# Kernel optimization log

Measured on AMD Instinct MI355X. Metric: run time of the kernel, lower is better.

Reference implementation:

```python
import jax, jax.numpy as jnp
import numpy as np

B = 4_000_000

# physical constants from initBatteryParams
R_ = 8.3144621
F_ = 96487.0
ALPHA = 0.5
SN = 0.0002
SP = 0.0002
KN = 20000.0
KP = 20000.0
VOL = 2.2e-05
VOLS = 0.1 * VOL
VOLB = VOL - VOLS
TO = 10.0
TSN = 90.0
TSP = 90.0
U0P = 4.03
U0N = 0.01
QMAX_BASE = 10000.0
RO_BASE = 10.0
T_DIFFUSION = 7.0e6  # repo default; attribute used in getNextState
DT = 1.0


def setup_inputs() -> dict:
    key = jax.random.key(0)
    ks = jax.random.split(key, 12)
    qMax = 1.4 * jnp.ones((B,), jnp.float32)   # 14000/qMaxBASE
    Ro = 0.015 * jnp.ones((B,), jnp.float32)   # 0.15/RoBASE
    # physically plausible initial state (get_initial_state) + small noise
    qM = qMax * QMAX_BASE  # [B]
    Tb = 292.1 + 0.5 * jax.random.normal(ks[0], (B, 1), jnp.float32)
    Vo = 0.01 * jax.random.uniform(ks[1], (B, 1), jnp.float32)
    Vsn = 0.01 * jax.random.uniform(ks[2], (B, 1), jnp.float32)
    Vsp = 0.01 * jax.random.uniform(ks[3], (B, 1), jnp.float32)
    jitter = lambda k: 1.0 + 0.01 * jax.random.normal(k, (B, 1), jnp.float32)
    qnB = (qM * 0.6 * VOLB / VOL)[:, None] * jitter(ks[4])
    qnS = (qM * 0.6 * VOLS / VOL)[:, None] * jitter(ks[5])
    qpB = (qM * 0.4 * VOLB / VOL)[:, None] * jitter(ks[6])
    qpS = (qM * 0.4 * VOLS / VOL)[:, None] * jitter(ks[7])
    states = jnp.concatenate([Tb, Vo, Vsn, Vsp, qnB, qnS, qpB, qpS], axis=1)
    inputs = 1.0 + 2.0 * jax.random.uniform(ks[8], (B, 1), jnp.float32)  # current [A]
    kw = jax.random.split(ks[9], 8)
    return {
        "inputs": inputs, "states": states, "qMax": qMax, "Ro": Ro,
        "Wp0": 0.5 * jax.random.normal(kw[0], (8, 1), jnp.float32),
        "bp0": 0.1 * jax.random.normal(kw[1], (8,), jnp.float32),
        "Wp2": 0.5 * jax.random.normal(kw[2], (4, 8), jnp.float32),
        "bp2": 0.1 * jax.random.normal(kw[3], (4,), jnp.float32),
        "Wp4": 0.5 * jax.random.normal(kw[4], (1, 4), jnp.float32),
        "bp4": 0.1 * jax.random.normal(kw[5], (1,), jnp.float32),
        "Wn": 0.0016 * jnp.ones((1, 1), jnp.float32),  # ~fitted Linear(1,1)
        "bn": -0.0008 * jnp.ones((1,), jnp.float32),
    }


def _mlp_p(x, Wp0, bp0, Wp2, bp2, Wp4, bp4):
    h = jnp.tanh(x @ Wp0.T + bp0)
    h = jnp.tanh(h @ Wp2.T + bp2)
    return h @ Wp4.T + bp4


def _cell(inputs, states, qMax, Ro, Wp0, bp0, Wp2, bp2, Wp4, bp4, Wn, bn):
    Tb, Vo, Vsn, Vsp, qnB, qnS, qpB, qpS = jnp.split(states, 8, axis=1)
    i = inputs  # [B,1]
    qSMax = (qMax * QMAX_BASE * VOLS / VOL)[:, None]  # [B,1]
    # --- getNextState ---
    xpS = jnp.clip(qpS / qSMax, 1e-18, 1.0)
    xnS = jnp.clip(qnS / qSMax, 1e-18, 1.0)
    Jn0 = 1e-18 + KN * (1.0 - xnS) ** ALPHA * xnS ** ALPHA
    Jp0 = 1e-18 + KP * (1.0 - xpS) ** ALPHA * xpS ** ALPHA
    qdotDiffusionBSn = (qnB / VOLB - qnS / VOLS) / T_DIFFUSION
    qdotDiffusionBSp = (qpB / VOLB - qpS / VOLS) / T_DIFFUSION
    Jn = i / SN
    Jp = i / SP
    VoNominal = i * Ro[:, None] * RO_BASE
    VsnNominal = R_ * Tb / F_ / ALPHA * jnp.arcsinh(Jn / (2.0 * Jn0))
    VspNominal = R_ * Tb / F_ / ALPHA * jnp.arcsinh(Jp / (2.0 * Jp0))
    Tb2 = Tb  # Tbdot = 0
    Vo2 = Vo + (VoNominal - Vo) / TO * DT
    Vsn2 = Vsn + (VsnNominal - Vsn) / TSN * DT
    Vsp2 = Vsp + (VspNominal - Vsp) / TSP * DT
    qnB2 = qnB + (-qdotDiffusionBSn) * DT
    qnS2 = qnS + (qdotDiffusionBSn - i) * DT
    qpB2 = qpB + (-qdotDiffusionBSp) * DT
    qpS2 = qpS + (i + qdotDiffusionBSp) * DT
    XNew = jnp.concatenate([Tb2, Vo2, Vsn2, Vsp2, qnB2, qnS2, qpB2, qpS2], axis=1)
    # --- getNextOutput (on XNew) ---
    xpS_o = qpS2 / qSMax
    xnS_o = qnS2 / qSMax
    VepMLP = _mlp_p(xpS_o, Wp0, bp0, Wp2, bp2, Wp4, bp4)
    VenMLP = xnS_o @ Wn.T + bn
    safe_log_p = jnp.clip((1.0 - xpS_o) / xpS_o, 1e-18, 1e18)
    safe_log_n = jnp.clip((1.0 - xnS_o) / xnS_o, 1e-18, 1e18)
    Vep = U0P + R_ * Tb2 / F_ * jnp.log(safe_log_p) + VepMLP
    Ven = U0N + R_ * Tb2 / F_ * jnp.log(safe_log_n) + VenMLP
    V = Vep - Ven - Vo2 - Vsn2 - Vsp2
    return V, XNew


def reference(inputs, states, qMax, Ro, Wp0, bp0, Wp2, bp2, Wp4, bp4, Wn, bn):
    return _cell(inputs, states, qMax, Ro, Wp0, bp0, Wp2, bp2, Wp4, bp4, Wn, bn)
```

## Files before the change

### kernel.cpp

```cpp
#include <hip/hip_runtime.h>
#include <math.h>

typedef float v4f __attribute__((ext_vector_type(4)));
typedef float v2f __attribute__((ext_vector_type(2)));

#define RTF       (8.3144621f / 96487.0f)
#define VOLS_     2.2e-06f
#define VOLB_     1.98e-05f
#define INV_TDIFF (1.0f / 7.0e6f)

#define LUT_N 4096
#define BLOCK 256
#define GRID  2048

__device__ __forceinline__ float asinh_pos(float x) {
    return __logf(x + sqrtf(fmaf(x, x, 1.0f)));
}

__device__ __forceinline__ float jval(float x) {
    float j0 = 1e-18f + 20000.0f * sqrtf(fmaxf(x * (1.0f - x), 0.0f));
    return 1.0f / (2.0f * j0);
}

__device__ __forceinline__ void mlp_log_eval(
    float x,
    const float* __restrict__ Wp0, const float* __restrict__ bp0,
    const float* __restrict__ Wp2, const float* __restrict__ bp2,
    const float* __restrict__ Wp4, const float* __restrict__ bp4,
    float* mlp_out, float* log_out)
{
    float h1[8];
#pragma unroll
    for (int j = 0; j < 8; j++)
        h1[j] = tanhf(fmaf(x, Wp0[j], bp0[j]));
    float mlp = bp4[0];
#pragma unroll
    for (int k = 0; k < 4; k++) {
        float a = bp2[k];
#pragma unroll
        for (int j = 0; j < 8; j++)
            a = fmaf(h1[j], Wp2[k * 8 + j], a);
        mlp = fmaf(tanhf(a), Wp4[k], mlp);
    }
    *mlp_out = mlp;
    float r = fminf(fmaxf((1.0f - x) / fmaxf(x, 1e-30f), 1e-18f), 1e18f);
    *log_out = RTF * logf(r);
}

__global__ __launch_bounds__(256) void build_lut_kernel(
    const float* __restrict__ Wp0, const float* __restrict__ bp0,
    const float* __restrict__ Wp2, const float* __restrict__ bp2,
    const float* __restrict__ Wp4, const float* __restrict__ bp4,
    v2f* __restrict__ lutJ2, v4f* __restrict__ lutO4)
{
    int idx = blockIdx.x * blockDim.x + threadIdx.x;
    if (idx >= LUT_N) return;
    const float dx = 1.0f / (float)(LUT_N - 1);
    float x0 = (float)idx * dx;
    float x1 = fminf(x0 + dx, 1.0f);

    v2f j; j.x = jval(x0); j.y = jval(x1);
    lutJ2[idx] = j;

    float m0, l0, m1, l1;
    mlp_log_eval(x0, Wp0, bp0, Wp2, bp2, Wp4, bp4, &m0, &l0);
    mlp_log_eval(x1, Wp0, bp0, Wp2, bp2, Wp4, bp4, &m1, &l1);
    v4f o; o.x = m0; o.y = l0; o.z = m1; o.w = l1;
    lutO4[idx] = o;
}

__global__ __launch_bounds__(BLOCK) void battery_cell_kernel(
    const float* __restrict__ inp,
    const float* __restrict__ st,
    const float* __restrict__ qMaxp,
    const float* __restrict__ Rop,
    const float* __restrict__ Wn,
    const float* __restrict__ bn,
    const v2f*   __restrict__ lutJ2,
    const v4f*   __restrict__ lutO4,
    float* __restrict__ outV,
    float* __restrict__ outX,
    int B)
{
    const v4f* st4 = (const v4f*)st;
    v4f* ox4 = (v4f*)outX;
    float wn = Wn[0], wbn = bn[0];

    int stride = GRID * BLOCK;
    for (int b = blockIdx.x * BLOCK + threadIdx.x; b < B; b += stride) {
        v4f s0 = st4[2 * b];
        v4f s1 = st4[2 * b + 1];
        float i  = inp[b];
        float qm = qMaxp[b];
        float ro = Rop[b];

        float Tb  = s0.x, Vo  = s0.y, Vsn = s0.z, Vsp = s0.w;
        float qnB = s1.x, qnS = s1.y, qpB = s1.z, qpS = s1.w;

        float invq = __fdividef(1.0f, qm * 1000.0f);

        float xpS = fminf(fmaxf(qpS * invq, 1e-18f), 1.0f);
        float xnS = fminf(fmaxf(qnS * invq, 1e-18f), 1.0f);

        float tn = xnS * (float)(LUT_N - 1);
        float tp = xpS * (float)(LUT_N - 1);
        int in0 = min((int)tn, LUT_N - 2);
        int ip0 = min((int)tp, LUT_N - 2);
        float fn = tn - (float)in0;
        float fp = tp - (float)ip0;
        v2f jn = lutJ2[in0];
        v2f jp = lutJ2[ip0];
        float inv2Jn = fmaf(fn, jn.y - jn.x, jn.x);
        float inv2Jp = fmaf(fp, jp.y - jp.x, jp.x);

        float qdotn = (qnB * (1.0f / VOLB_) - qnS * (1.0f / VOLS_)) * INV_TDIFF;
        float qdotp = (qpB * (1.0f / VOLB_) - qpS * (1.0f / VOLS_)) * INV_TDIFF;

        float Jn     = i * 5000.0f;
        float VoNom  = i * ro * 10.0f;
        float coef   = RTF * Tb * 2.0f;
        float VsnNom = coef * asinh_pos(Jn * inv2Jn);
        float VspNom = coef * asinh_pos(Jn * inv2Jp);

        float Vo2  = Vo  + (VoNom  - Vo ) * 0.1f;
        float Vsn2 = Vsn + (VsnNom - Vsn) * (1.0f / 90.0f);
        float Vsp2 = Vsp + (VspNom - Vsp) * (1.0f / 90.0f);
        float qnB2 = qnB - qdotn;
        float qnS2 = qnS + qdotn - i;
        float qpB2 = qpB - qdotp;
        float qpS2 = qpS + i + qdotp;

        float xp = qpS2 * invq;
        float xn = qnS2 * invq;

        float tpo = fminf(fmaxf(xp, 0.0f), 1.0f) * (float)(LUT_N - 1);
        float tno = fminf(fmaxf(xn, 0.0f), 1.0f) * (float)(LUT_N - 1);
        int ipo = min((int)tpo, LUT_N - 2);
        int ino = min((int)tno, LUT_N - 2);
        float fpo = tpo - (float)ipo;
        float fno = tno - (float)ino;
        v4f op = lutO4[ipo];
        v4f on = lutO4[ino];
        float mlp_p = fmaf(fpo, op.z - op.x, op.x);
        float log_p = fmaf(fpo, op.w - op.y, op.y);
        float log_n = fmaf(fno, on.w - on.y, on.y);

        float Vep = 4.03f + Tb * log_p + mlp_p;
        float Ven = 0.01f + Tb * log_n + fmaf(xn, wn, wbn);
        float V = Vep - Ven - Vo2 - Vsn2 - Vsp2;

        outV[b] = V;
        v4f o0; o0.x = Tb;   o0.y = Vo2;  o0.z = Vsn2; o0.w = Vsp2;
        v4f o1; o1.x = qnB2; o1.y = qnS2; o1.z = qpB2; o1.w = qpS2;
        ox4[2 * b]     = o0;
        ox4[2 * b + 1] = o1;
    }
}

extern "C" void kernel_launch(void* const* d_in, const int* in_sizes, int n_in,
                              void* d_out, int out_size, void* d_ws, size_t ws_size,
                              hipStream_t stream) {
    const float* inp  = (const float*)d_in[0];
    const float* st   = (const float*)d_in[1];
    const float* qMax = (const float*)d_in[2];
    const float* Ro   = (const float*)d_in[3];
    const float* Wp0  = (const float*)d_in[4];
    const float* bp0  = (const float*)d_in[5];
    const float* Wp2  = (const float*)d_in[6];
    const float* bp2  = (const float*)d_in[7];
    const float* Wp4  = (const float*)d_in[8];
    const float* bp4  = (const float*)d_in[9];
    const float* Wn   = (const float*)d_in[10];
    const float* bn   = (const float*)d_in[11];

    int B = in_sizes[0];
    float* outV = (float*)d_out;
    float* outX = (float*)d_out + B;

    v2f* lutJ2 = (v2f*)d_ws;
    v4f* lutO4 = (v4f*)((char*)d_ws + LUT_N * 8);

    build_lut_kernel<<<LUT_N / 256, 256, 0, stream>>>(
        Wp0, bp0, Wp2, bp2, Wp4, bp4, lutJ2, lutO4);

    battery_cell_kernel<<<GRID, BLOCK, 0, stream>>>(
        inp, st, qMax, Ro, Wn, bn, lutJ2, lutO4, outV, outX, B);
}
```

Baseline: 308.0 us.

## Stage state rows through swizzled LDS for fully coalesced loads and stores

Each block now loads its 256 state rows (two float4 each) into shared memory with contiguous per-thread float4 accesses, then reads them back per row through an XOR swizzle. Outputs are staged back through LDS the same way before being written. This removes the stride-2 float4 global access pattern. The persistent grid-stride loop is replaced by one thread per row with a full-size grid. The cost is two barriers per block, extra LDS traffic, and a separate fallback path for the tail block.

```diff
diff --git a/kernel.cpp b/kernel.cpp
--- a/kernel.cpp
+++ b/kernel.cpp
@@ -11,11 +11,12 @@
 
 #define LUT_N 4096
 #define BLOCK 256
-#define GRID  2048
 
 __device__ __forceinline__ float asinh_pos(float x) {
     return __logf(x + sqrtf(fmaf(x, x, 1.0f)));
 }
+
+__device__ __forceinline__ int swz(int c) { return c ^ ((c >> 1) & 7); }
 
 __device__ __forceinline__ float jval(float x) {
     float j0 = 1e-18f + 20000.0f * sqrtf(fmaxf(x * (1.0f - x), 0.0f));
@@ -69,6 +70,71 @@
     lutO4[idx] = o;
 }
 
+__device__ __forceinline__ void process_row(
+    v4f s0, v4f s1, float i, float qm, float ro,
+    float wn, float wbn,
+    const v2f* __restrict__ lutJ2, const v4f* __restrict__ lutO4,
+    float& Vout, v4f& o0, v4f& o1)
+{
+    float Tb  = s0.x, Vo  = s0.y, Vsn = s0.z, Vsp = s0.w;
+    float qnB = s1.x, qnS = s1.y, qpB = s1.z, qpS = s1.w;
+
+    float invq = __fdividef(1.0f, qm * 1000.0f);
+
+    float xpS = fminf(fmaxf(qpS * invq, 1e-18f), 1.0f);
+    float xnS = fminf(fmaxf(qnS * invq, 1e-18f), 1.0f);
+
+    float tn = xnS * (float)(LUT_N - 1);
+    float tp = xpS * (float)(LUT_N - 1);
+    int in0 = min((int)tn, LUT_N - 2);
+    int ip0 = min((int)tp, LUT_N - 2);
+    float fn = tn - (float)in0;
+    float fp = tp - (float)ip0;
+    v2f jn = lutJ2[in0];
+    v2f jp = lutJ2[ip0];
+    float inv2Jn = fmaf(fn, jn.y - jn.x, jn.x);
+    float inv2Jp = fmaf(fp, jp.y - jp.x, jp.x);
+
+    float qdotn = (qnB * (1.0f / VOLB_) - qnS * (1.0f / VOLS_)) * INV_TDIFF;
+    float qdotp = (qpB * (1.0f / VOLB_) - qpS * (1.0f / VOLS_)) * INV_TDIFF;
+
+    float Jn     = i * 5000.0f;
+    float VoNom  = i * ro * 10.0f;
+    float coef   = RTF * Tb * 2.0f;
+    float VsnNom = coef * asinh_pos(Jn * inv2Jn);
+    float VspNom = coef * asinh_pos(Jn * inv2Jp);
+
+    float Vo2  = Vo  + (VoNom  - Vo ) * 0.1f;
+    float Vsn2 = Vsn + (VsnNom - Vsn) * (1.0f / 90.0f);
+    float Vsp2 = Vsp + (VspNom - Vsp) * (1.0f / 90.0f);
+    float qnB2 = qnB - qdotn;
+    float qnS2 = qnS + qdotn - i;
+    float qpB2 = qpB - qdotp;
+    float qpS2 = qpS + i + qdotp;
+
+    float xp = qpS2 * invq;
+    float xn = qnS2 * invq;
+
+    float tpo = fminf(fmaxf(xp, 0.0f), 1.0f) * (float)(LUT_N - 1);
+    float tno = fminf(fmaxf(xn, 0.0f), 1.0f) * (float)(LUT_N - 1);
+    int ipo = min((int)tpo, LUT_N - 2);
+    int ino = min((int)tno, LUT_N - 2);
+    float fpo = tpo - (float)ipo;
+    float fno = tno - (float)ino;
+    v4f op = lutO4[ipo];
+    v4f on = lutO4[ino];
+    float mlp_p = fmaf(fpo, op.z - op.x, op.x);
+    float log_p = fmaf(fpo, op.w - op.y, op.y);
+    float log_n = fmaf(fno, on.w - on.y, on.y);
+
+    float Vep = 4.03f + Tb * log_p + mlp_p;
+    float Ven = 0.01f + Tb * log_n + fmaf(xn, wn, wbn);
+    Vout = Vep - Ven - Vo2 - Vsn2 - Vsp2;
+
+    o0.x = Tb;   o0.y = Vo2;  o0.z = Vsn2; o0.w = Vsp2;
+    o1.x = qnB2; o1.y = qnS2; o1.z = qpB2; o1.w = qpS2;
+}
+
 __global__ __launch_bounds__(BLOCK) void battery_cell_kernel(
     const float* __restrict__ inp,
     const float* __restrict__ st,
@@ -82,78 +148,53 @@
     float* __restrict__ outX,
     int B)
 {
-    const v4f* st4 = (const v4f*)st;
-    v4f* ox4 = (v4f*)outX;
+    __shared__ v4f ldsA[2 * BLOCK];
+    __shared__ v4f ldsB[2 * BLOCK];
+
+    int tid  = threadIdx.x;
+    int base = blockIdx.x * BLOCK;
     float wn = Wn[0], wbn = bn[0];
 
-    int stride = GRID * BLOCK;
-    for (int b = blockIdx.x * BLOCK + threadIdx.x; b < B; b += stride) {
-        v4f s0 = st4[2 * b];
-        v4f s1 = st4[2 * b + 1];
+    if (base + BLOCK <= B) {
+        int b = base + tid;
         float i  = inp[b];
         float qm = qMaxp[b];
         float ro = Rop[b];
 
-        float Tb  = s0.x, Vo  = s0.y, Vsn = s0.z, Vsp = s0.w;
-        float qnB = s1.x, qnS = s1.y, qpB = s1.z, qpS = s1.w;
-
-        float invq = __fdividef(1.0f, qm * 1000.0f);
-
-        float xpS = fminf(fmaxf(qpS * invq, 1e-18f), 1.0f);
-        float xnS = fminf(fmaxf(qnS * invq, 1e-18f), 1.0f);
-
-        float tn = xnS * (float)(LUT_N - 1);
-        float tp = xpS * (float)(LUT_N - 1);
-        int in0 = min((int)tn, LUT_N - 2);
-        int ip0 = min((int)tp, LUT_N - 2);
-        float fn = tn - (float)in0;
-        float fp = tp - (float)ip0;
-        v2f jn = lutJ2[in0];
-        v2f jp = lutJ2[ip0];
-        float inv2Jn = fmaf(fn, jn.y - jn.x, jn.x);
-        float inv2Jp = fmaf(fp, jp.y - jp.x, jp.x);
-
-        float qdotn = (qnB * (1.0f / VOLB_) - qnS * (1.0f / VOLS_)) * INV_TDIFF;
-        float qdotp = (qpB * (1.0f / VOLB_) - qpS * (1.0f / VOLS_)) * INV_TDIFF;
-
-        float Jn     = i * 5000.0f;
-        float VoNom  = i * ro * 10.0f;
-        float coef   = RTF * Tb * 2.0f;
-        float VsnNom = coef * asinh_pos(Jn * inv2Jn);
-        float VspNom = coef * asinh_pos(Jn * inv2Jp);
-
-        float Vo2  = Vo  + (VoNom  - Vo ) * 0.1f;
-        float Vsn2 = Vsn + (VsnNom - Vsn) * (1.0f / 90.0f);
-        float Vsp2 = Vsp + (VspNom - Vsp) * (1.0f / 90.0f);
-        float qnB2 = qnB - qdotn;
-        float qnS2 = qnS + qdotn - i;
-        float qpB2 = qpB - qdotp;
-        float qpS2 = qpS + i + qdotp;
-
-        float xp = qpS2 * invq;
-        float xn = qnS2 * invq;
-
-        float tpo = fminf(fmaxf(xp, 0.0f), 1.0f) * (float)(LUT_N - 1);
-        float tno = fminf(fmaxf(xn, 0.0f), 1.0f) * (float)(LUT_N - 1);
-        int ipo = min((int)tpo, LUT_N - 2);
-        int ino = min((int)tno, LUT_N - 2);
-        float fpo = tpo - (float)ipo;
-        float fno = tno - (float)ino;
-        v4f op = lutO4[ipo];
-        v4f on = lutO4[ino];
-        float mlp_p = fmaf(fpo, op.z - op.x, op.x);
-        float log_p = fmaf(fpo, op.w - op.y, op.y);
-        float log_n = fmaf(fno, on.w - on.y, on.y);
-
-        float Vep = 4.03f + Tb * log_p + mlp_p;
-        float Ven = 0.01f + Tb * log_n + fmaf(xn, wn, wbn);
-        float V = Vep - Ven - Vo2 - Vsn2 - Vsp2;
+        const v4f* stG = (const v4f*)st + 2 * base;
+        ldsA[swz(tid)]         = stG[tid];
+        ldsA[swz(tid + BLOCK)] = stG[tid + BLOCK];
+        __syncthreads();
+
+        v4f s0 = ldsA[swz(2 * tid)];
+        v4f s1 = ldsA[swz(2 * tid + 1)];
+
+        float V; v4f o0, o1;
+        process_row(s0, s1, i, qm, ro, wn, wbn, lutJ2, lutO4, V, o0, o1);
 
         outV[b] = V;
-        v4f o0; o0.x = Tb;   o0.y = Vo2;  o0.z = Vsn2; o0.w = Vsp2;
-        v4f o1; o1.x = qnB2; o1.y = qnS2; o1.z = qpB2; o1.w = qpS2;
-        ox4[2 * b]     = o0;
-        ox4[2 * b + 1] = o1;
+
+        ldsB[swz(2 * tid)]     = o0;
+        ldsB[swz(2 * tid + 1)] = o1;
+        __syncthreads();
+
+        v4f* oxG = (v4f*)outX + 2 * base;
+        oxG[tid]         = ldsB[swz(tid)];
+        oxG[tid + BLOCK] = ldsB[swz(tid + BLOCK)];
+    } else {
+        int b = base + tid;
+        if (b < B) {
+            const v4f* st4 = (const v4f*)st;
+            v4f s0 = st4[2 * b];
+            v4f s1 = st4[2 * b + 1];
+            float V; v4f o0, o1;
+            process_row(s0, s1, inp[b], qMaxp[b], Rop[b], wn, wbn,
+                        lutJ2, lutO4, V, o0, o1);
+            outV[b] = V;
+            v4f* ox4 = (v4f*)outX;
+            ox4[2 * b]     = o0;
+            ox4[2 * b + 1] = o1;
+        }
     }
 }
 
@@ -183,6 +224,7 @@
     build_lut_kernel<<<LUT_N / 256, 256, 0, stream>>>(
         Wp0, bp0, Wp2, bp2, Wp4, bp4, lutJ2, lutO4);
 
-    battery_cell_kernel<<<GRID, BLOCK, 0, stream>>>(
+    int grid = (B + BLOCK - 1) / BLOCK;
+    battery_cell_kernel<<<grid, BLOCK, 0, stream>>>(
         inp, st, qMax, Ro, Wn, bn, lutJ2, lutO4, outV, outX, B);
 }
```

Result: faster. 293.3 us (-4.8%).
